# Kernel tuning notes

Hardware: AMD Instinct MI355X
Metric: run time of the kernel (lower is better)

## Reference

```python
import jax, jax.numpy as jnp
import numpy as np

B, T, D, H = 4, 2048, 1024, 16
HD = D // H

def setup_inputs() -> dict:
    key = jax.random.key(0)
    ks = jax.random.split(key, 12)
    s = 0.02
    return {
        "query": jax.random.normal(ks[0], (B, T, D), dtype=jnp.float32),
        "key_": jax.random.normal(ks[1], (B, T, D), dtype=jnp.float32),
        "value": jax.random.normal(ks[2], (B, T, D), dtype=jnp.float32),
        "attention_mask": jnp.zeros((B, T, T), dtype=bool),
        "Wq": jax.random.normal(ks[3], (D, D), dtype=jnp.float32) * s,
        "bq": jnp.zeros((D,), dtype=jnp.float32),
        "Wk": jax.random.normal(ks[4], (D, D), dtype=jnp.float32) * s,
        "bk": jnp.zeros((D,), dtype=jnp.float32),
        "Wv": jax.random.normal(ks[5], (D, D), dtype=jnp.float32) * s,
        "bv": jnp.zeros((D,), dtype=jnp.float32),
        "Wo": jax.random.normal(ks[6], (D, D), dtype=jnp.float32) * s,
        "bo": jnp.zeros((D,), dtype=jnp.float32),
    }

def reference(query, key_, value, attention_mask, Wq, bq, Wk, bk, Wv, bv, Wo, bo):
    scale = 1.0 / jnp.sqrt(jnp.float32(HD))
    # projections (torch Linear: x @ W.T + b), split heads -> [B, H, T, HD]
    q = (query @ Wq.T + bq).reshape(B, T, H, HD).transpose(0, 2, 1, 3)
    k = (key_ @ Wk.T + bk).reshape(B, T, H, HD).transpose(0, 2, 1, 3)
    v = (value @ Wv.T + bv).reshape(B, T, H, HD).transpose(0, 2, 1, 3)
    scores = jnp.einsum('bhqd,bhkd->bhqk', q, k) * scale  # [B,H,T,T]
    mask = attention_mask[:, None, :, :]  # [B,1,T,T], True = masked
    scores = jnp.where(mask, -jnp.inf, scores)
    attn = jax.nn.softmax(scores, axis=-1)
    out = jnp.einsum('bhqk,bhkd->bhqd', attn, v)  # [B,H,T,HD]
    out = out.transpose(0, 2, 1, 3).reshape(B, T, D)
    return out @ Wo.T + bo
```

## Files before the change

### kernel.cpp

```cpp
#include <hip/hip_runtime.h>
#include <hip/hip_bf16.h>
#include <math.h>


typedef short bf16x8 __attribute__((ext_vector_type(8)));
typedef short bf16x4 __attribute__((ext_vector_type(4)));
typedef float f32x4  __attribute__((ext_vector_type(4)));
typedef float f32x16 __attribute__((ext_vector_type(16)));
typedef unsigned u32x4v __attribute__((ext_vector_type(4)));

#define DEV __device__ __forceinline__

DEV short f2bf(float f) {
    union { float f; unsigned u; } x; x.f = f;
    unsigned r = x.u + 0x7fffu + ((x.u >> 16) & 1u);
    return (short)(r >> 16);
}

DEV unsigned cvtpk(float lo, float hi) {
    unsigned r;
    asm("v_cvt_pk_bf16_f32 %0, %1, %2" : "=v"(r) : "v"(lo), "v"(hi));
    return r;
}

DEV void pl32swap(unsigned &a, unsigned &b) {
    asm volatile("v_permlane32_swap_b32 %0, %1" : "+v"(a), "+v"(b));
}

DEV float fexp2(float x) {
    float r;
    asm("v_exp_f32 %0, %1\n\ts_nop 0" : "=v"(r) : "v"(x));
    return r;
}

DEV void gload16(const void* g, void* lds_wave_base) {
    __builtin_amdgcn_global_load_lds(
        (const __attribute__((address_space(1))) void*)g,
        (__attribute__((address_space(3))) void*)lds_wave_base, 16, 0, 0);
}

DEV void barrier_pinned() {
    __builtin_amdgcn_sched_barrier(0);
    __builtin_amdgcn_s_barrier();
    __builtin_amdgcn_sched_barrier(0);
}

DEV f32x4 mfma16(bf16x8 a, bf16x8 b, f32x4 c) {
    return __builtin_amdgcn_mfma_f32_16x16x32_bf16(a, b, c, 0, 0, 0);
}
DEV f32x16 mfma32(bf16x8 a, bf16x8 b, f32x16 c) {
    return __builtin_amdgcn_mfma_f32_32x32x16_bf16(a, b, c, 0, 0, 0);
}

__global__ __launch_bounds__(256) void cvt_w4(
    const float* __restrict__ a, const float* __restrict__ b,
    const float* __restrict__ c, const float* __restrict__ d,
    short* __restrict__ oa, short* __restrict__ ob,
    short* __restrict__ oc, short* __restrict__ od) {
    const int sel = blockIdx.x >> 9;
    const float* in = sel == 0 ? a : sel == 1 ? b : sel == 2 ? c : d;
    short* out      = sel == 0 ? oa : sel == 1 ? ob : sel == 2 ? oc : od;
    int i = ((blockIdx.x & 511) * 256 + threadIdx.x) * 8;
    f32x4 x = *(const f32x4*)(in + i);
    f32x4 y = *(const f32x4*)(in + i + 4);
    union { unsigned u[4]; bf16x8 v; } p;
    p.u[0] = cvtpk(x[0], x[1]); p.u[1] = cvtpk(x[2], x[3]);
    p.u[2] = cvtpk(y[0], y[1]); p.u[3] = cvtpk(y[2], y[3]);
    *(bf16x8*)(out + i) = p.v;
}

__global__ __launch_bounds__(256, 2) void gemm_qkv4(
    const float* __restrict__ Aq, const float* __restrict__ Ak, const float* __restrict__ Av,
    const short* __restrict__ Wqb, const short* __restrict__ Wkb, const short* __restrict__ Wvb,
    const float* __restrict__ bqp, const float* __restrict__ bkp, const float* __restrict__ bvp,
    short* __restrict__ Qo, short* __restrict__ Ko, short* __restrict__ Vo, float qscale)
{
    __shared__ float Alds[2][4096];
    __shared__ short Blds[2][8192];

    const int t = threadIdx.x, wave = t >> 6, lane = t & 63;
    const int lr = lane & 15, lg = lane >> 4;
    const int raw = blockIdx.x;
    const int wg = (raw & 7) * 96 + (raw >> 3);
    const int sel = wg >> 8, inner = wg & 255;
    const int m0 = (inner >> 2) * 128, n0 = (inner & 3) * 256;
    const int wr = wave >> 1, wc = wave & 1;

    const float* A    = sel == 0 ? Aq  : sel == 1 ? Ak  : Av;
    const short* W    = sel == 0 ? Wqb : sel == 1 ? Wkb : Wvb;
    const float* bias = sel == 0 ? bqp : sel == 1 ? bkp : bvp;

    const float* Asrc0; const float* Asrc1; const float* Asrc2; const float* Asrc3;
    {
        auto mk = [&](int i) {
            const int p = i * 256 + t, kq = p >> 8, cp = p & 255;
            const int rp = cp >> 1, pc = cp & 1, cpair = pc ^ ((rp >> 3) & 1);
            return A + (size_t)(m0 + rp) * 1024 + kq * 8 + cpair * 4;
        };
        Asrc0 = mk(0); Asrc1 = mk(1); Asrc2 = mk(2); Asrc3 = mk(3);
    }
    const short* Wsrc = W + (size_t)(n0 + t) * 1024;

    auto stage = [&](float* dA, short* dB, int k0) {
        gload16(Asrc0 + k0, (char*)dA +         wave * 1024);
        gload16(Asrc1 + k0, (char*)dA +  4096 + wave * 1024);
        gload16(Asrc2 + k0, (char*)dA +  8192 + wave * 1024);
        gload16(Asrc3 + k0, (char*)dA + 12288 + wave * 1024);
        gload16(Wsrc + k0,      (char*)dB +         wave * 1024);
        gload16(Wsrc + k0 + 8,  (char*)dB +  4096 + wave * 1024);
        gload16(Wsrc + k0 + 16, (char*)dB +  8192 + wave * 1024);
        gload16(Wsrc + k0 + 24, (char*)dB + 12288 + wave * 1024);
    };

    const int s16 = (lr >> 3) & 1;
    const int aBase = lg * 1024 + (wr * 64 + lr) * 8;
    const int loOff = aBase + s16 * 4;
    const int hiOff = aBase + (s16 ^ 1) * 4;

    f32x4 acc[4][8] = {};
    stage(Alds[0], Blds[0], 0);

    auto kstep = [&](int ts, int BUF) {
        if (ts < 31) {
            stage(Alds[BUF ^ 1], Blds[BUF ^ 1], (ts + 1) * 32);
            asm volatile("s_waitcnt vmcnt(8)" ::: "memory");
        } else {
            asm volatile("s_waitcnt vmcnt(0)" ::: "memory");
        }
        barrier_pinned();
        bf16x8 af[4];
        #pragma unroll
        for (int mi = 0; mi < 4; mi++) {
            f32x4 lo = *(const f32x4*)(&Alds[BUF][0] + loOff + mi * 128);
            f32x4 hi = *(const f32x4*)(&Alds[BUF][0] + hiOff + mi * 128);
            union { unsigned u[4]; bf16x8 v; } pa;
            pa.u[0] = cvtpk(lo[0], lo[1]); pa.u[1] = cvtpk(lo[2], lo[3]);
            pa.u[2] = cvtpk(hi[0], hi[1]); pa.u[3] = cvtpk(hi[2], hi[3]);
            af[mi] = pa.v;
        }
        #pragma unroll
        for (int ni = 0; ni < 8; ni++) {
            bf16x8 bfr = *(const bf16x8*)(&Blds[BUF][0] + lg * 2048
                                          + (wc * 128 + ni * 16 + lr) * 8);
            #pragma unroll
            for (int mi = 0; mi < 4; mi++)
                acc[mi][ni] = mfma16(af[mi], bfr, acc[mi][ni]);
        }
        barrier_pinned();
    };

    #pragma unroll 1
    for (int it = 0; it < 16; ++it) { kstep(2 * it, 0); kstep(2 * it + 1, 1); }

    #pragma unroll
    for (int mi = 0; mi < 4; mi++) {
        #pragma unroll
        for (int ni = 0; ni < 8; ni++) {
            const int n      = n0 + wc * 128 + ni * 16 + lr;
            const int m_base = m0 + wr * 64 + mi * 16 + lg * 4;
            const float bv   = bias[n];
            f32x4 a = acc[mi][ni];
            if (sel == 2) {
                const int bb = m_base >> 11, tt = m_base & 2047;
                bf16x4 p;
                #pragma unroll
                for (int r = 0; r < 4; r++) p[r] = f2bf(a[r] + bv);
                *(bf16x4*)(Vo + (size_t)bb * 2097152 + (size_t)n * 2048 + tt) = p;
            } else {
                short* C = sel ? Ko : Qo;
                const float sc = sel ? 1.0f : qscale;
                #pragma unroll
                for (int r = 0; r < 4; r++)
                    C[(size_t)(m_base + r) * 1024 + n] = f2bf((a[r] + bv) * sc);
            }
        }
    }
}

__global__ __launch_bounds__(256) void gemm_out64(
    const short* __restrict__ A, const short* __restrict__ W,
    const float* __restrict__ bias, float* __restrict__ C)
{
    __shared__ short Alds[2][8192];
    __shared__ short Blds[2][8192];

    const int t = threadIdx.x;
    const int wave = t >> 6, lane = t & 63;
    const int lr = lane & 15, lg = lane >> 4;
    const int wg = (blockIdx.x & 7) * 64 + (blockIdx.x >> 3);
    const int m0 = (wg >> 3) * 128, n0 = (wg & 7) * 128;
    const int wr = wave >> 1, wc = wave & 1;

    const int kb0 = t >> 7, r0 = t & 127;
    const short* As = A + (size_t)(m0 + r0) * 1024 + kb0 * 8;
    const short* Ws = W + (size_t)(n0 + r0) * 1024 + kb0 * 8;

    auto stage = [&](short* dA, short* dB, int k0) {
        #pragma unroll
        for (int i = 0; i < 4; i++) {
            gload16(As + k0 + i * 16, (char*)dA + i * 4096 + wave * 1024);
            gload16(Ws + k0 + i * 16, (char*)dB + i * 4096 + wave * 1024);
        }
    };

    f32x4 acc[4][4] = {};
    stage(Alds[0], Blds[0], 0);

    auto kstep = [&](int ts, int BUF) {
        if (ts < 15) {
            stage(Alds[BUF ^ 1], Blds[BUF ^ 1], (ts + 1) * 64);
            asm volatile("s_waitcnt vmcnt(8)" ::: "memory");
        } else {
            asm volatile("s_waitcnt vmcnt(0)" ::: "memory");
        }
        barrier_pinned();
        #pragma unroll
        for (int kk = 0; kk < 2; kk++) {
            bf16x8 af[4], bfr[4];
            #pragma unroll
            for (int mi = 0; mi < 4; mi++)
                af[mi] = *(const bf16x8*)(Alds[BUF] + (kk * 4 + lg) * 1024
                                          + (wr * 64 + mi * 16 + lr) * 8);
            #pragma unroll
            for (int ni = 0; ni < 4; ni++)
                bfr[ni] = *(const bf16x8*)(Blds[BUF] + (kk * 4 + lg) * 1024
                                           + (wc * 64 + ni * 16 + lr) * 8);
            #pragma unroll
            for (int mi = 0; mi < 4; mi++)
                #pragma unroll
                for (int ni = 0; ni < 4; ni++)
                    acc[mi][ni] = mfma16(af[mi], bfr[ni], acc[mi][ni]);
        }
        barrier_pinned();
    };

    #pragma unroll 1
    for (int it = 0; it < 8; ++it) { kstep(2 * it, 0); kstep(2 * it + 1, 1); }

    #pragma unroll
    for (int mi = 0; mi < 4; mi++) {
        #pragma unroll
        for (int ni = 0; ni < 4; ni++) {
            const int n      = n0 + wc * 64 + ni * 16 + lr;
            const int m_base = m0 + wr * 64 + mi * 16 + lg * 4;
            const float bv   = bias[n];
            f32x4 a = acc[mi][ni];
            #pragma unroll
            for (int r = 0; r < 4; r++)
                C[(size_t)(m_base + r) * 1024 + n] = a[r] + bv;
        }
    }
}

__global__ __launch_bounds__(256) void mask_scan(const unsigned char* __restrict__ mask,
                                                 unsigned char* __restrict__ flags) {
    __shared__ int anyk[32];
    const int t = threadIdx.x, kt = t & 31, g = t >> 5;
    const int b = blockIdx.x >> 6, qt = blockIdx.x & 63;
    if (t < 32) anyk[t] = 0;
    __syncthreads();
    unsigned acc = 0;
    const unsigned char* base = mask + ((size_t)b * 2048 + qt * 32 + g * 4) * 2048 + kt * 64;
    #pragma unroll
    for (int rr = 0; rr < 4; rr++) {
        const uint4* p = (const uint4*)(base + (size_t)rr * 2048);
        #pragma unroll
        for (int s = 0; s < 4; s++) { uint4 v = p[s]; acc |= v.x | v.y | v.z | v.w; }
    }
    if (acc) anyk[kt] = 1;
    __syncthreads();
    if (t < 32) flags[((size_t)b * 64 + qt) * 32 + t] = (unsigned char)anyk[t];
}

__global__ __launch_bounds__(256, 2) void attn_fwd5(
    const short* __restrict__ Q, const short* __restrict__ K,
    const short* __restrict__ Vt, const unsigned char* __restrict__ mask,
    const unsigned char* __restrict__ flags, short* __restrict__ O)
{
    __shared__ short lds[2][2][8192];

    const int t = threadIdx.x, wave = t >> 6, lane = t & 63;
    const int j31 = lane & 31, hi = lane >> 5;

    const int raw = blockIdx.x;
    const int wg  = (raw & 7) * 128 + (raw >> 3);
    const int qblk = wg & 15, bh = wg >> 4;
    const int h = bh & 15, b = bh >> 4;
    const int q0 = qblk * 128 + wave * 32;

    bf16x8 qf[4];
    {
        const short* qp = Q + ((size_t)b * 2048 + q0 + j31) * 1024 + h * 64 + hi * 8;
        #pragma unroll
        for (int ck = 0; ck < 4; ck++) qf[ck] = *(const bf16x8*)(qp + ck * 16);
    }
    unsigned long long fmask;
    {
        unsigned char fb = flags[((size_t)b * 64 + qblk * 4 + wave) * 32 + j31];
        fmask = __ballot(fb != 0);
    }
    bf16x8 onesv;
    #pragma unroll
    for (int i = 0; i < 8; i++) onesv[i] = (short)0x3F80;

    const short* Kg = K + ((size_t)b * 2048) * 1024 + h * 64;
    const short* Vg = Vt + (size_t)b * 2097152 + (size_t)h * 64 * 2048;

    auto stage = [&](short* dK, short* dV, int tk) {
        #pragma unroll
        for (int i = 0; i < 4; i++) {
            const int s = i * 256 + t;
            const int rK = s >> 3, cK = ((s & 7) ^ (rK & 7)) * 8;
            gload16(Kg + (size_t)(tk + rK) * 1024 + cK, dK + i * 2048 + wave * 512);
            const int rV = s >> 4, cV = ((s & 15) ^ (rV & 15)) * 8;
            gload16(Vg + (size_t)rV * 2048 + tk + cV, dV + i * 2048 + wave * 512);
        }
    };

    stage(&lds[0][0][0], &lds[0][1][0], 0);

    f32x16 oA = {}, oB = {}, accL = {};
    float m = -1e30f;
    const int swk = j31 & 7, swv = j31 & 15;

    auto tile = [&](int J, int BUF) {
        if (J < 15) {
            stage(&lds[BUF ^ 1][0][0], &lds[BUF ^ 1][1][0], (J + 1) * 128);
            asm volatile("s_waitcnt vmcnt(8)" ::: "memory");
        } else {
            asm volatile("s_waitcnt vmcnt(0)" ::: "memory");
        }
        barrier_pinned();
        const short* ldsK = &lds[BUF][0][0];
        const short* ldsV = &lds[BUF][1][0];
        const bool masked = ((fmask >> (2 * J)) & 3ULL) != 0;

        f32x16 sA = {}, sB = {};
        __builtin_amdgcn_s_setprio(1);
        #pragma unroll
        for (int ck = 0; ck < 4; ck++) {
            const int co = ((2 * ck + hi) ^ swk) * 8;
            bf16x8 k0 = *(const bf16x8*)(ldsK + (j31      ) * 64 + co);
            bf16x8 k1 = *(const bf16x8*)(ldsK + (32 + j31) * 64 + co);
            sA = mfma32(k0, qf[ck], sA);
            sB = mfma32(k1, qf[ck], sB);
        }
        __builtin_amdgcn_s_setprio(0);
        if (masked) {
            const unsigned char* mp = mask + ((size_t)b * 2048 + q0 + j31) * 2048
                                           + (size_t)J * 128 + hi * 4;
            #pragma unroll
            for (int rg = 0; rg < 4; rg++) {
                unsigned ma = *(const unsigned*)(mp + rg * 8);
                unsigned mb = *(const unsigned*)(mp + 32 + rg * 8);
                #pragma unroll
                for (int e = 0; e < 4; e++) {
                    if ((ma >> (8 * e)) & 0xFFu) sA[rg * 4 + e] = -1e30f;
                    if ((mb >> (8 * e)) & 0xFFu) sB[rg * 4 + e] = -1e30f;
                }
            }
        }
        float tmab = fmaxf(sA[0], sA[1]);
        #pragma unroll
        for (int r = 2; r < 16; r += 2) tmab = fmaxf(fmaxf(tmab, sA[r]), sA[r + 1]);
        #pragma unroll
        for (int r = 0; r < 16; r += 2) tmab = fmaxf(fmaxf(tmab, sB[r]), sB[r + 1]);
        f32x16 pA, pB;
        #pragma unroll
        for (int r = 0; r < 16; r++) { pA[r] = fexp2(sA[r] - m); pB[r] = fexp2(sB[r] - m); }

        f32x16 sC = {}, sD = {};
        #pragma unroll
        for (int ck = 0; ck < 4; ck++) {
            const int co = ((2 * ck + hi) ^ swk) * 8;
            bf16x8 k2 = *(const bf16x8*)(ldsK + (64 + j31) * 64 + co);
            bf16x8 k3 = *(const bf16x8*)(ldsK + (96 + j31) * 64 + co);
            sC = mfma32(k2, qf[ck], sC);
            sD = mfma32(k3, qf[ck], sD);
        }
        if (masked) {
            const unsigned char* mp = mask + ((size_t)b * 2048 + q0 + j31) * 2048
                                           + (size_t)J * 128 + hi * 4;
            #pragma unroll
            for (int rg = 0; rg < 4; rg++) {
                unsigned mc = *(const unsigned*)(mp + 64 + rg * 8);
                unsigned md = *(const unsigned*)(mp + 96 + rg * 8);
                #pragma unroll
                for (int e = 0; e < 4; e++) {
                    if ((mc >> (8 * e)) & 0xFFu) sC[rg * 4 + e] = -1e30f;
                    if ((md >> (8 * e)) & 0xFFu) sD[rg * 4 + e] = -1e30f;
                }
            }
        }
        float tm = tmab;
        #pragma unroll
        for (int r = 0; r < 16; r += 2) tm = fmaxf(fmaxf(tm, sC[r]), sC[r + 1]);
        #pragma unroll
        for (int r = 0; r < 16; r += 2) tm = fmaxf(fmaxf(tm, sD[r]), sD[r + 1]);
        tm = fmaxf(tm, __shfl_xor(tm, 32));
        if (!__all(tm <= m + 8.f)) {
            const float mnew = fmaxf(m, tm);
            const float fs = fexp2(m - mnew);
            m = mnew;
            #pragma unroll
            for (int r = 0; r < 16; r++) { pA[r] = fexp2(sA[r] - m); pB[r] = fexp2(sB[r] - m); }
            #pragma unroll
            for (int r = 0; r < 16; r++) { oA[r] *= fs; oB[r] *= fs; }
            accL[0] *= fs;
        }
        #pragma unroll
        for (int r = 0; r < 16; r++) { sC[r] = fexp2(sC[r] - m); sD[r] = fexp2(sD[r] - m); }

        __builtin_amdgcn_s_setprio(1);
        #pragma unroll
        for (int c = 0; c < 8; c++) {
            const f32x16& sX = (c < 2) ? pA : (c < 4) ? pB : (c < 6) ? sC : sD;
            const int rb = 8 * (c & 1);
            unsigned A0 = cvtpk(sX[rb],     sX[rb + 1]), B0 = cvtpk(sX[rb + 4], sX[rb + 5]);
            unsigned A1 = cvtpk(sX[rb + 2], sX[rb + 3]), B1 = cvtpk(sX[rb + 6], sX[rb + 7]);
            pl32swap(A0, B0); pl32swap(A1, B1);
            union { unsigned u[4]; bf16x8 v; } pu;
            pu.u[0] = A0; pu.u[1] = A1; pu.u[2] = B0; pu.u[3] = B1;
            const int co = ((2 * c + hi) ^ swv) * 8;
            bf16x8 v0 = *(const bf16x8*)(ldsV + (j31      ) * 128 + co);
            bf16x8 v1 = *(const bf16x8*)(ldsV + (32 + j31) * 128 + co);
            oA   = mfma32(v0, pu.v, oA);
            oB   = mfma32(v1, pu.v, oB);
            accL = mfma32(onesv, pu.v, accL);
        }
        __builtin_amdgcn_s_setprio(0);
        barrier_pinned();
    };

    #pragma unroll 1
    for (int jj = 0; jj < 8; ++jj) { tile(2 * jj, 0); tile(2 * jj + 1, 1); }

    __syncthreads();
    unsigned* ow = (unsigned*)&lds[0][0][0] + wave * (32 * 34);
    const float inv = 1.f / accL[0];
    #pragma unroll
    for (int o = 0; o < 2; o++)
        #pragma unroll
        for (int rp = 0; rp < 8; rp++) {
            const int r  = 2 * rp;
            const int hd = 2 * (rp & 1) + 8 * (rp >> 1) + 4 * hi + 32 * o;
            const float v0 = (o ? oB[r]     : oA[r])     * inv;
            const float v1 = (o ? oB[r + 1] : oA[r + 1]) * inv;
            ow[j31 * 34 + (hd >> 1)] = cvtpk(v0, v1);
        }
    __syncthreads();
    {
        const size_t orow = ((size_t)b * 2048 + q0 + j31) * 1024 + h * 64 + hi * 32;
        unsigned* gout = (unsigned*)(O + orow);
        const unsigned* src = ow + j31 * 34 + hi * 16;
        #pragma unroll
        for (int i = 0; i < 4; i++) {
            u32x4v v;
            v[0] = src[i*4]; v[1] = src[i*4+1]; v[2] = src[i*4+2]; v[3] = src[i*4+3];
            *(u32x4v*)(gout + i * 4) = v;
        }
    }
}

extern "C" void kernel_launch(void* const* d_in, const int* in_sizes, int n_in,
                              void* d_out, int out_size, void* d_ws, size_t ws_size,
                              hipStream_t stream)
{
    const float* query = (const float*)d_in[0];
    const float* key_  = (const float*)d_in[1];
    const float* value = (const float*)d_in[2];
    const unsigned char* amask = (const unsigned char*)d_in[3];
    const float* Wq = (const float*)d_in[4];
    const float* bq = (const float*)d_in[5];
    const float* Wk = (const float*)d_in[6];
    const float* bk = (const float*)d_in[7];
    const float* Wv = (const float*)d_in[8];
    const float* bv = (const float*)d_in[9];
    const float* Wo = (const float*)d_in[10];
    const float* bo = (const float*)d_in[11];
    float* out = (float*)d_out;

    char* ws = (char*)d_ws;
    const size_t MB = 1024 * 1024;
    short* Wqb = (short*)(ws + 0 * MB);
    short* Wkb = (short*)(ws + 2 * MB);
    short* Wvb = (short*)(ws + 4 * MB);
    short* Wob = (short*)(ws + 6 * MB);
    short* Qb  = (short*)(ws + 8 * MB);
    short* Kb  = (short*)(ws + 24 * MB);
    short* Vtb = (short*)(ws + 40 * MB);
    short* Xb  = (short*)(ws + 56 * MB);
    unsigned char* flagsb = (unsigned char*)(ws + 0 * MB);

    cvt_w4<<<2048, 256, 0, stream>>>(Wq, Wk, Wv, Wo, Wqb, Wkb, Wvb, Wob);

    const float qscale = 0.125f * 1.44269504088896f;
    gemm_qkv4<<<768, 256, 0, stream>>>(query, key_, value, Wqb, Wkb, Wvb,
                                       bq, bk, bv, Qb, Kb, Vtb, qscale);

    mask_scan<<<256, 256, 0, stream>>>(amask, flagsb);

    attn_fwd5<<<1024, 256, 0, stream>>>(Qb, Kb, Vtb, amask, flagsb, Xb);

    gemm_out64<<<512, 256, 0, stream>>>(Xb, Wob, bo, out);
}
```

Before: 251.2 us.

## Halve attention KV tile to 64 keys, raise occupancy, compute row-sum with VALU

The attention kernel now processes 64-key tiles instead of 128, halving LDS use and register pressure so launch bounds can target 4 workgroups per CU instead of 2. The softmax denominator is accumulated with scalar adds and a cross-half shuffle, replacing the extra ones-vector MFMA per PV step. Online-softmax rescaling is simplified because each tile has only two score blocks. In exchange there are twice as many tiles, so more barriers and more per-tile max/rescale overhead.

```diff
diff --git a/kernel.cpp b/kernel.cpp
--- a/kernel.cpp
+++ b/kernel.cpp
@@ -272,12 +272,12 @@
     if (t < 32) flags[((size_t)b * 64 + qt) * 32 + t] = (unsigned char)anyk[t];
 }
 
-__global__ __launch_bounds__(256, 2) void attn_fwd5(
+__global__ __launch_bounds__(256, 4) void attn_fwd6(
     const short* __restrict__ Q, const short* __restrict__ K,
     const short* __restrict__ Vt, const unsigned char* __restrict__ mask,
     const unsigned char* __restrict__ flags, short* __restrict__ O)
 {
-    __shared__ short lds[2][2][8192];
+    __shared__ short lds[2][2][4096];
 
     const int t = threadIdx.x, wave = t >> 6, lane = t & 63;
     const int j31 = lane & 31, hi = lane >> 5;
@@ -299,145 +299,114 @@
         unsigned char fb = flags[((size_t)b * 64 + qblk * 4 + wave) * 32 + j31];
         fmask = __ballot(fb != 0);
     }
-    bf16x8 onesv;
-    #pragma unroll
-    for (int i = 0; i < 8; i++) onesv[i] = (short)0x3F80;
 
     const short* Kg = K + ((size_t)b * 2048) * 1024 + h * 64;
     const short* Vg = Vt + (size_t)b * 2097152 + (size_t)h * 64 * 2048;
 
     auto stage = [&](short* dK, short* dV, int tk) {
         #pragma unroll
-        for (int i = 0; i < 4; i++) {
+        for (int i = 0; i < 2; i++) {
             const int s = i * 256 + t;
-            const int rK = s >> 3, cK = ((s & 7) ^ (rK & 7)) * 8;
-            gload16(Kg + (size_t)(tk + rK) * 1024 + cK, dK + i * 2048 + wave * 512);
-            const int rV = s >> 4, cV = ((s & 15) ^ (rV & 15)) * 8;
-            gload16(Vg + (size_t)rV * 2048 + tk + cV, dV + i * 2048 + wave * 512);
+            const int r = s >> 3, cs = ((s & 7) ^ (r & 7)) * 8;
+            gload16(Kg + (size_t)(tk + r) * 1024 + cs, dK + i * 2048 + wave * 512);
+            gload16(Vg + (size_t)r * 2048 + tk + cs, dV + i * 2048 + wave * 512);
         }
     };
 
     stage(&lds[0][0][0], &lds[0][1][0], 0);
 
-    f32x16 oA = {}, oB = {}, accL = {};
-    float m = -1e30f;
-    const int swk = j31 & 7, swv = j31 & 15;
+    f32x16 oA = {}, oB = {};
+    float m = -1e30f, l = 0.f;
+    const int sw = j31 & 7;
 
     auto tile = [&](int J, int BUF) {
-        if (J < 15) {
-            stage(&lds[BUF ^ 1][0][0], &lds[BUF ^ 1][1][0], (J + 1) * 128);
-            asm volatile("s_waitcnt vmcnt(8)" ::: "memory");
+        if (J < 31) {
+            stage(&lds[BUF ^ 1][0][0], &lds[BUF ^ 1][1][0], (J + 1) * 64);
+            asm volatile("s_waitcnt vmcnt(4)" ::: "memory");
         } else {
             asm volatile("s_waitcnt vmcnt(0)" ::: "memory");
         }
         barrier_pinned();
         const short* ldsK = &lds[BUF][0][0];
         const short* ldsV = &lds[BUF][1][0];
-        const bool masked = ((fmask >> (2 * J)) & 3ULL) != 0;
 
         f32x16 sA = {}, sB = {};
         __builtin_amdgcn_s_setprio(1);
         #pragma unroll
         for (int ck = 0; ck < 4; ck++) {
-            const int co = ((2 * ck + hi) ^ swk) * 8;
+            const int co = ((2 * ck + hi) ^ sw) * 8;
             bf16x8 k0 = *(const bf16x8*)(ldsK + (j31      ) * 64 + co);
             bf16x8 k1 = *(const bf16x8*)(ldsK + (32 + j31) * 64 + co);
             sA = mfma32(k0, qf[ck], sA);
             sB = mfma32(k1, qf[ck], sB);
         }
         __builtin_amdgcn_s_setprio(0);
-        if (masked) {
+
+        if ((fmask >> J) & 1ULL) {
             const unsigned char* mp = mask + ((size_t)b * 2048 + q0 + j31) * 2048
-                                           + (size_t)J * 128 + hi * 4;
-            #pragma unroll
-            for (int rg = 0; rg < 4; rg++) {
-                unsigned ma = *(const unsigned*)(mp + rg * 8);
-                unsigned mb = *(const unsigned*)(mp + 32 + rg * 8);
+                                           + (size_t)J * 64 + hi * 4;
+            #pragma unroll
+            for (int a2 = 0; a2 < 2; a2++)
                 #pragma unroll
-                for (int e = 0; e < 4; e++) {
-                    if ((ma >> (8 * e)) & 0xFFu) sA[rg * 4 + e] = -1e30f;
-                    if ((mb >> (8 * e)) & 0xFFu) sB[rg * 4 + e] = -1e30f;
+                for (int rg = 0; rg < 4; rg++) {
+                    unsigned mb = *(const unsigned*)(mp + a2 * 32 + rg * 8);
+                    #pragma unroll
+                    for (int e = 0; e < 4; e++) {
+                        if ((mb >> (8 * e)) & 0xFFu) {
+                            if (a2 == 0) sA[rg * 4 + e] = -1e30f;
+                            else         sB[rg * 4 + e] = -1e30f;
+                        }
+                    }
                 }
-            }
-        }
-        float tmab = fmaxf(sA[0], sA[1]);
-        #pragma unroll
-        for (int r = 2; r < 16; r += 2) tmab = fmaxf(fmaxf(tmab, sA[r]), sA[r + 1]);
-        #pragma unroll
-        for (int r = 0; r < 16; r += 2) tmab = fmaxf(fmaxf(tmab, sB[r]), sB[r + 1]);
-        f32x16 pA, pB;
-        #pragma unroll
-        for (int r = 0; r < 16; r++) { pA[r] = fexp2(sA[r] - m); pB[r] = fexp2(sB[r] - m); }
-
-        f32x16 sC = {}, sD = {};
-        #pragma unroll
-        for (int ck = 0; ck < 4; ck++) {
-            const int co = ((2 * ck + hi) ^ swk) * 8;
-            bf16x8 k2 = *(const bf16x8*)(ldsK + (64 + j31) * 64 + co);
-            bf16x8 k3 = *(const bf16x8*)(ldsK + (96 + j31) * 64 + co);
-            sC = mfma32(k2, qf[ck], sC);
-            sD = mfma32(k3, qf[ck], sD);
-        }
-        if (masked) {
-            const unsigned char* mp = mask + ((size_t)b * 2048 + q0 + j31) * 2048
-                                           + (size_t)J * 128 + hi * 4;
-            #pragma unroll
-            for (int rg = 0; rg < 4; rg++) {
-                unsigned mc = *(const unsigned*)(mp + 64 + rg * 8);
-                unsigned md = *(const unsigned*)(mp + 96 + rg * 8);
-                #pragma unroll
-                for (int e = 0; e < 4; e++) {
-                    if ((mc >> (8 * e)) & 0xFFu) sC[rg * 4 + e] = -1e30f;
-                    if ((md >> (8 * e)) & 0xFFu) sD[rg * 4 + e] = -1e30f;
-                }
-            }
-        }
-        float tm = tmab;
-        #pragma unroll
-        for (int r = 0; r < 16; r += 2) tm = fmaxf(fmaxf(tm, sC[r]), sC[r + 1]);
-        #pragma unroll
-        for (int r = 0; r < 16; r += 2) tm = fmaxf(fmaxf(tm, sD[r]), sD[r + 1]);
+        }
+
+        float tm = fmaxf(sA[0], sA[1]);
+        #pragma unroll
+        for (int r = 2; r < 16; r += 2) tm = fmaxf(fmaxf(tm, sA[r]), sA[r + 1]);
+        #pragma unroll
+        for (int r = 0; r < 16; r += 2) tm = fmaxf(fmaxf(tm, sB[r]), sB[r + 1]);
         tm = fmaxf(tm, __shfl_xor(tm, 32));
         if (!__all(tm <= m + 8.f)) {
             const float mnew = fmaxf(m, tm);
             const float fs = fexp2(m - mnew);
-            m = mnew;
-            #pragma unroll
-            for (int r = 0; r < 16; r++) { pA[r] = fexp2(sA[r] - m); pB[r] = fexp2(sB[r] - m); }
+            m = mnew; l *= fs;
             #pragma unroll
             for (int r = 0; r < 16; r++) { oA[r] *= fs; oB[r] *= fs; }
-            accL[0] *= fs;
-        }
-        #pragma unroll
-        for (int r = 0; r < 16; r++) { sC[r] = fexp2(sC[r] - m); sD[r] = fexp2(sD[r] - m); }
+        }
+        float ps = 0.f;
+        #pragma unroll
+        for (int r = 0; r < 16; r++) { sA[r] = fexp2(sA[r] - m); ps += sA[r]; }
+        #pragma unroll
+        for (int r = 0; r < 16; r++) { sB[r] = fexp2(sB[r] - m); ps += sB[r]; }
+        ps += __shfl_xor(ps, 32);
+        l += ps;
 
         __builtin_amdgcn_s_setprio(1);
         #pragma unroll
-        for (int c = 0; c < 8; c++) {
-            const f32x16& sX = (c < 2) ? pA : (c < 4) ? pB : (c < 6) ? sC : sD;
+        for (int c = 0; c < 4; c++) {
+            const f32x16& sX = (c < 2) ? sA : sB;
             const int rb = 8 * (c & 1);
             unsigned A0 = cvtpk(sX[rb],     sX[rb + 1]), B0 = cvtpk(sX[rb + 4], sX[rb + 5]);
             unsigned A1 = cvtpk(sX[rb + 2], sX[rb + 3]), B1 = cvtpk(sX[rb + 6], sX[rb + 7]);
             pl32swap(A0, B0); pl32swap(A1, B1);
             union { unsigned u[4]; bf16x8 v; } pu;
             pu.u[0] = A0; pu.u[1] = A1; pu.u[2] = B0; pu.u[3] = B1;
-            const int co = ((2 * c + hi) ^ swv) * 8;
-            bf16x8 v0 = *(const bf16x8*)(ldsV + (j31      ) * 128 + co);
-            bf16x8 v1 = *(const bf16x8*)(ldsV + (32 + j31) * 128 + co);
-            oA   = mfma32(v0, pu.v, oA);
-            oB   = mfma32(v1, pu.v, oB);
-            accL = mfma32(onesv, pu.v, accL);
+            const int co = ((2 * c + hi) ^ sw) * 8;
+            bf16x8 v0 = *(const bf16x8*)(ldsV + (j31      ) * 64 + co);
+            bf16x8 v1 = *(const bf16x8*)(ldsV + (32 + j31) * 64 + co);
+            oA = mfma32(v0, pu.v, oA);
+            oB = mfma32(v1, pu.v, oB);
         }
         __builtin_amdgcn_s_setprio(0);
         barrier_pinned();
     };
 
     #pragma unroll 1
-    for (int jj = 0; jj < 8; ++jj) { tile(2 * jj, 0); tile(2 * jj + 1, 1); }
+    for (int jj = 0; jj < 16; ++jj) { tile(2 * jj, 0); tile(2 * jj + 1, 1); }
 
     __syncthreads();
     unsigned* ow = (unsigned*)&lds[0][0][0] + wave * (32 * 34);
-    const float inv = 1.f / accL[0];
+    const float inv = 1.f / l;
     #pragma unroll
     for (int o = 0; o < 2; o++)
         #pragma unroll
@@ -500,7 +469,7 @@
 
     mask_scan<<<256, 256, 0, stream>>>(amask, flagsb);
 
-    attn_fwd5<<<1024, 256, 0, stream>>>(Qb, Kb, Vtb, amask, flagsb, Xb);
+    attn_fwd6<<<1024, 256, 0, stream>>>(Qb, Kb, Vtb, amask, flagsb, Xb);
 
     gemm_out64<<<512, 256, 0, stream>>>(Xb, Wob, bo, out);
 }
```

Result: no change. 251.9 us (+0.3%).
